# Optimization experiments

Hardware: AMD Instinct MI355X
Metric: run time of the kernel (lower is better)

Reference implementation:

```python
import jax, jax.numpy as jnp
import numpy as np

N_NODES = 100_000
N_EDGES = 1_600_000
F_NODE = 4
F_EDGE = 5
H = 64
EDGE_DIM = 2 * H + F_EDGE  # 133


def setup_inputs() -> dict:
    key = jax.random.key(0)
    ks = jax.random.split(key, 24)
    s = 0.05
    inp = {
        "node_feat": jax.random.normal(ks[0], (N_NODES, F_NODE), jnp.float32),
        "edge_feat": jax.random.normal(ks[1], (N_EDGES, F_EDGE), jnp.float32),
        "src": jax.random.randint(ks[2], (N_EDGES,), 0, N_NODES, jnp.int32),
        "dst": jax.random.randint(ks[3], (N_EDGES,), 0, N_NODES, jnp.int32),
        # SAGEConv 1 (DGL mean aggregator: fc_self(h) + fc_neigh(mean_neigh(h)) + bias)
        "W1s": jax.random.normal(ks[4], (F_NODE, H), jnp.float32) * s,
        "W1n": jax.random.normal(ks[5], (F_NODE, H), jnp.float32) * s,
        "b1": jnp.zeros((H,), jnp.float32),
        # SAGEConv 2
        "W2s": jax.random.normal(ks[6], (H, H), jnp.float32) * s,
        "W2n": jax.random.normal(ks[7], (H, H), jnp.float32) * s,
        "b2": jnp.zeros((H,), jnp.float32),
        # nodeprocess: Linear(F_NODE? no -> applied to h which is H-dim) Linear(H? )
        # NOTE: original declares nn.Linear(num_node_features, hidden) but applies it to h (H-dim);
        # we follow the applied shape, Linear(H, H), so the math is runnable and consistent.
        "Wnp": jax.random.normal(ks[8], (H, H), jnp.float32) * s,
        "bnp": jnp.zeros((H,), jnp.float32),
        # edgeprocess: Linear(EDGE_DIM, H) -> tanh -> Linear(H, 1)
        "We1": jax.random.normal(ks[9], (EDGE_DIM, H), jnp.float32) * s,
        "be1": jnp.zeros((H,), jnp.float32),
        "We2": jax.random.normal(ks[10], (H, 1), jnp.float32) * s,
        "be2": jnp.zeros((1,), jnp.float32),
        # lin1: Linear(EDGE_DIM, H); lin2: Linear(H, 1)
        "Wl1": jax.random.normal(ks[11], (EDGE_DIM, H), jnp.float32) * s,
        "bl1": jnp.zeros((H,), jnp.float32),
        "Wl2": jax.random.normal(ks[12], (H, 1), jnp.float32) * s,
        "bl2": jnp.zeros((1,), jnp.float32),
    }
    return inp


def _sage_mean(h, src, dst, Ws, Wn, b, inv_deg):
    # project first (cheaper: N x d instead of E x d), then gather+scatter-mean
    msg = (h @ Wn)[src]                                    # [E, H]
    agg = jax.ops.segment_sum(msg, dst, num_segments=h.shape[0]) * inv_deg
    return h @ Ws + agg + b


def reference(node_feat, edge_feat, src, dst,
              W1s, W1n, b1, W2s, W2n, b2,
              Wnp, bnp, We1, be1, We2, be2,
              Wl1, bl1, Wl2, bl2):
    n = node_feat.shape[0]
    deg = jax.ops.segment_sum(jnp.ones_like(dst, jnp.float32), dst, num_segments=n)
    inv_deg = (1.0 / jnp.maximum(deg, 1.0))[:, None]       # [N,1]

    h = jax.nn.relu(_sage_mean(node_feat, src, dst, W1s, W1n, b1, inv_deg))
    h = jax.nn.relu(_sage_mean(h, src, dst, W2s, W2n, b2, inv_deg))

    h_src = jax.nn.relu(h[src] @ Wnp + bnp)                # [E, H]
    h_dst = jax.nn.relu(h[dst] @ Wnp + bnp)                # [E, H]
    ef = jnp.concatenate([h_src, h_dst, edge_feat], axis=1)  # [E, 133]

    w = jax.nn.sigmoid(jnp.tanh(ef @ We1 + be1) @ We2 + be2)  # [E, 1]
    efw = ef * w
    out = jax.nn.relu(efw @ Wl1 + bl1)                     # dropout: eval mode (identity)
    return out @ Wl2 + bl2                                 # [E, 1]
```

## Files before the change

kernel.cpp:

```cpp
#include <hip/hip_runtime.h>
#include <math.h>


__device__ __forceinline__ float fast_tanh(float x) {
    x = fminf(fmaxf(x, -15.f), 15.f);
    float e2 = __expf(2.f * x);
    return (e2 - 1.f) * __builtin_amdgcn_rcpf(e2 + 1.f);
}
__device__ __forceinline__ float fast_sigmoid(float x) {
    x = fminf(fmaxf(x, -60.f), 60.f);
    return __builtin_amdgcn_rcpf(1.f + __expf(-x));
}
__device__ __forceinline__ unsigned short f2bf(float f) {
    unsigned u = __float_as_uint(f);
    u = u + 0x7FFFu + ((u >> 16) & 1u);
    return (unsigned short)(u >> 16);
}
__device__ __forceinline__ unsigned pack2bf(float lo, float hi) {
    return ((unsigned)f2bf(hi) << 16) | (unsigned)f2bf(lo);
}
__device__ __forceinline__ float bflo(unsigned u) { return __uint_as_float(u << 16); }
__device__ __forceinline__ float bfhi(unsigned u) { return __uint_as_float(u & 0xFFFF0000u); }

__device__ __forceinline__ float dpp_sum16(float x) {
    int t;
    t = __builtin_amdgcn_update_dpp(0, __float_as_int(x), 0xB1, 0xF, 0xF, true);
    x += __int_as_float(t);
    t = __builtin_amdgcn_update_dpp(0, __float_as_int(x), 0x4E, 0xF, 0xF, true);
    x += __int_as_float(t);
    t = __builtin_amdgcn_update_dpp(0, __float_as_int(x), 0x141, 0xF, 0xF, true);
    x += __int_as_float(t);
    t = __builtin_amdgcn_update_dpp(0, __float_as_int(x), 0x140, 0xF, 0xF, true);
    x += __int_as_float(t);
    return x;
}

__global__ void rank_k(const int* __restrict__ dst, int* __restrict__ deg,
                       int* __restrict__ rank, int E) {
    int e = blockIdx.x * blockDim.x + threadIdx.x;
    if (e < E) rank[e] = atomicAdd(&deg[dst[e]], 1);
}

__global__ void scan1_k(const int* __restrict__ deg, int* __restrict__ off,
                        int* __restrict__ bsum, int N) {
    __shared__ int tmp[256];
    int i = blockIdx.x * 256 + threadIdx.x;
    int v = (i < N) ? deg[i] : 0;
    tmp[threadIdx.x] = v;
    __syncthreads();
#pragma unroll
    for (int s = 1; s < 256; s <<= 1) {
        int t = (threadIdx.x >= s) ? tmp[threadIdx.x - s] : 0;
        __syncthreads();
        tmp[threadIdx.x] += t;
        __syncthreads();
    }
    if (i < N) off[i] = tmp[threadIdx.x] - v;
    if (threadIdx.x == 255) bsum[blockIdx.x] = tmp[255];
}

__global__ void scan2_k(int* __restrict__ bsum, int nb) {
    __shared__ int tmp[512];
    int i = threadIdx.x;
    int v = (i < nb) ? bsum[i] : 0;
    tmp[i] = v;
    __syncthreads();
#pragma unroll
    for (int s = 1; s < 512; s <<= 1) {
        int t = (i >= s) ? tmp[i - s] : 0;
        __syncthreads();
        tmp[i] += t;
        __syncthreads();
    }
    if (i < nb) bsum[i] = tmp[i] - v;
}

__global__ void scan3_k(int* __restrict__ off, const int* __restrict__ bsum,
                        int N, int E) {
    int i = blockIdx.x * 256 + threadIdx.x;
    if (i < N) off[i] += bsum[blockIdx.x];
    if (i == 0) off[N] = E;
}

__global__ void fill2_k(const int* __restrict__ src, const int* __restrict__ dst,
                        const int* __restrict__ off, const int* __restrict__ rank,
                        int2* __restrict__ csr, int E) {
    int e = blockIdx.x * blockDim.x + threadIdx.x;
    if (e >= E) return;
    csr[off[dst[e]] + rank[e]] = make_int2(src[e], e);
}

__global__ __launch_bounds__(256, 8)
void aggh1f_k(const int* __restrict__ off, const int2* __restrict__ csr,
              const float* __restrict__ nf,
              const float* __restrict__ W1s, const float* __restrict__ W1n,
              const float* __restrict__ b1, unsigned* __restrict__ h1b, int N) {
    int n = blockIdx.x * 16 + (threadIdx.x >> 4);
    if (n >= N) return;
    int q = threadIdx.x & 15;
    int s0 = off[n], s1 = off[n + 1];
    float4 a = {0.f, 0.f, 0.f, 0.f};
    for (int i = s0 + q; i < s1; i += 16) {
        float4 r = ((const float4*)nf)[csr[i].x];
        a.x += r.x; a.y += r.y; a.z += r.z; a.w += r.w;
    }
    a.x = dpp_sum16(a.x);
    a.y = dpp_sum16(a.y);
    a.z = dpp_sum16(a.z);
    a.w = dpp_sum16(a.w);
    float invd = 1.f / fmaxf((float)(s1 - s0), 1.f);
    a.x *= invd; a.y *= invd; a.z *= invd; a.w *= invd;
    float4 r = ((const float4*)nf)[n];
    const int j0 = q << 2;
    float4 acc = *(const float4*)&b1[j0];
#pragma unroll
    for (int k = 0; k < 4; ++k) {
        float rk = (k == 0) ? r.x : (k == 1) ? r.y : (k == 2) ? r.z : r.w;
        float ak = (k == 0) ? a.x : (k == 1) ? a.y : (k == 2) ? a.z : a.w;
        float4 ws = *(const float4*)&W1s[k * 64 + j0];
        float4 wn = *(const float4*)&W1n[k * 64 + j0];
        acc.x = fmaf(rk, ws.x, acc.x); acc.y = fmaf(rk, ws.y, acc.y);
        acc.z = fmaf(rk, ws.z, acc.z); acc.w = fmaf(rk, ws.w, acc.w);
        acc.x = fmaf(ak, wn.x, acc.x); acc.y = fmaf(ak, wn.y, acc.y);
        acc.z = fmaf(ak, wn.z, acc.z); acc.w = fmaf(ak, wn.w, acc.w);
    }
    uint2 pk;
    pk.x = pack2bf(fmaxf(acc.x, 0.f), fmaxf(acc.y, 0.f));
    pk.y = pack2bf(fmaxf(acc.z, 0.f), fmaxf(acc.w, 0.f));
    *(uint2*)&h1b[(size_t)n * 32 + (q << 1)] = pk;
}

__global__ __launch_bounds__(256, 8)
void gatherh1_k(const int* __restrict__ off, const int2* __restrict__ csr,
                const uint4* __restrict__ h1b4, uint4* __restrict__ ah1b4, int N) {
    int n = blockIdx.x * 4 + (threadIdx.x >> 6);
    if (n >= N) return;
    int l = threadIdx.x & 63;
    int g = l >> 3, q = l & 7;
    int s0 = off[n], s1 = off[n + 1];
    float a0 = 0.f, a1 = 0.f, a2 = 0.f, a3 = 0.f;
    float a4 = 0.f, a5 = 0.f, a6 = 0.f, a7 = 0.f;
    int i = s0;
    for (; i + 16 <= s1; i += 16) {
        int r0 = csr[i + g].x;
        int r1 = csr[i + 8 + g].x;
        uint4 v0 = h1b4[(size_t)r0 * 8 + q];
        uint4 v1 = h1b4[(size_t)r1 * 8 + q];
        a0 += bflo(v0.x) + bflo(v1.x); a1 += bfhi(v0.x) + bfhi(v1.x);
        a2 += bflo(v0.y) + bflo(v1.y); a3 += bfhi(v0.y) + bfhi(v1.y);
        a4 += bflo(v0.z) + bflo(v1.z); a5 += bfhi(v0.z) + bfhi(v1.z);
        a6 += bflo(v0.w) + bflo(v1.w); a7 += bfhi(v0.w) + bfhi(v1.w);
    }
    for (; i + 8 <= s1; i += 8) {
        int r = csr[i + g].x;
        uint4 v = h1b4[(size_t)r * 8 + q];
        a0 += bflo(v.x); a1 += bfhi(v.x);
        a2 += bflo(v.y); a3 += bfhi(v.y);
        a4 += bflo(v.z); a5 += bfhi(v.z);
        a6 += bflo(v.w); a7 += bfhi(v.w);
    }
    int rem = s1 - i;
    if (g < rem) {
        int r = csr[i + g].x;
        uint4 v = h1b4[(size_t)r * 8 + q];
        a0 += bflo(v.x); a1 += bfhi(v.x);
        a2 += bflo(v.y); a3 += bfhi(v.y);
        a4 += bflo(v.z); a5 += bfhi(v.z);
        a6 += bflo(v.w); a7 += bfhi(v.w);
    }
#pragma unroll
    for (int m = 8; m <= 32; m <<= 1) {
        a0 += __shfl_xor(a0, m); a1 += __shfl_xor(a1, m);
        a2 += __shfl_xor(a2, m); a3 += __shfl_xor(a3, m);
        a4 += __shfl_xor(a4, m); a5 += __shfl_xor(a5, m);
        a6 += __shfl_xor(a6, m); a7 += __shfl_xor(a7, m);
    }
    if (l < 8) {
        float invd = 1.f / fmaxf((float)(s1 - s0), 1.f);
        uint4 pk;
        pk.x = pack2bf(a0 * invd, a1 * invd);
        pk.y = pack2bf(a2 * invd, a3 * invd);
        pk.z = pack2bf(a4 * invd, a5 * invd);
        pk.w = pack2bf(a6 * invd, a7 * invd);
        ah1b4[(size_t)n * 8 + q] = pk;
    }
}

__device__ __forceinline__ void mac64(const float (*hT)[68], const float (*wt)[64],
                                      int rr, int cr, float acc[4][4]) {
#pragma unroll 8
    for (int k = 0; k < 64; ++k) {
        float4 a = *(const float4*)&hT[k][rr];
        float4 w = *(const float4*)&wt[k][cr];
        acc[0][0] = fmaf(a.x, w.x, acc[0][0]); acc[0][1] = fmaf(a.x, w.y, acc[0][1]);
        acc[0][2] = fmaf(a.x, w.z, acc[0][2]); acc[0][3] = fmaf(a.x, w.w, acc[0][3]);
        acc[1][0] = fmaf(a.y, w.x, acc[1][0]); acc[1][1] = fmaf(a.y, w.y, acc[1][1]);
        acc[1][2] = fmaf(a.y, w.z, acc[1][2]); acc[1][3] = fmaf(a.y, w.w, acc[1][3]);
        acc[2][0] = fmaf(a.z, w.x, acc[2][0]); acc[2][1] = fmaf(a.z, w.y, acc[2][1]);
        acc[2][2] = fmaf(a.z, w.z, acc[2][2]); acc[2][3] = fmaf(a.z, w.w, acc[2][3]);
        acc[3][0] = fmaf(a.w, w.x, acc[3][0]); acc[3][1] = fmaf(a.w, w.y, acc[3][1]);
        acc[3][2] = fmaf(a.w, w.z, acc[3][2]); acc[3][3] = fmaf(a.w, w.w, acc[3][3]);
    }
}

__global__ __launch_bounds__(256, 4)
void node_mlp_k(const unsigned* __restrict__ h1b, const unsigned* __restrict__ ah1b,
                const float* __restrict__ W2s, const float* __restrict__ W2n,
                const float* __restrict__ b2, const float* __restrict__ Wnp,
                const float* __restrict__ bnp, const float* __restrict__ We1,
                const float* __restrict__ Wl1, unsigned short* __restrict__ ST, int N) {
    __shared__ __align__(16) float hT[64][68];
    __shared__ __align__(16) float wt[64][64];
    const int t = threadIdx.x;
    const int m0 = blockIdx.x * 64;
    const int cr = (t & 15) << 2, rr = (t >> 4) << 2;
    float acc[4][4] = {};

#pragma unroll
    for (int it = 0; it < 8; ++it) {
        int u = it * 256 + t;
        int m = u >> 5, p = u & 31;
        int row = m0 + m;
        unsigned v = (row < N) ? h1b[(size_t)row * 32 + p] : 0u;
        hT[2 * p][m] = bflo(v);
        hT[2 * p + 1][m] = bfhi(v);
    }
#pragma unroll
    for (int it = 0; it < 16; ++it) {
        int k = it * 4 + (t >> 6), c = t & 63;
        wt[k][c] = W2s[k * 64 + c];
    }
    __syncthreads();
    mac64(hT, wt, rr, cr, acc);
    __syncthreads();

#pragma unroll
    for (int it = 0; it < 8; ++it) {
        int u = it * 256 + t;
        int m = u >> 5, p = u & 31;
        int row = m0 + m;
        unsigned v = (row < N) ? ah1b[(size_t)row * 32 + p] : 0u;
        hT[2 * p][m] = bflo(v);
        hT[2 * p + 1][m] = bfhi(v);
    }
#pragma unroll
    for (int it = 0; it < 16; ++it) {
        int k = it * 4 + (t >> 6), c = t & 63;
        wt[k][c] = W2n[k * 64 + c];
    }
    __syncthreads();
    mac64(hT, wt, rr, cr, acc);
    __syncthreads();

#pragma unroll
    for (int i = 0; i < 4; ++i)
#pragma unroll
        for (int q = 0; q < 4; ++q)
            hT[cr + q][rr + i] = fmaxf(acc[i][q] + b2[cr + q], 0.f);
#pragma unroll
    for (int it = 0; it < 16; ++it) {
        int k = it * 4 + (t >> 6), c = t & 63;
        wt[k][c] = Wnp[k * 64 + c];
    }
    __syncthreads();
    float ac2[4][4] = {};
    mac64(hT, wt, rr, cr, ac2);
    __syncthreads();

#pragma unroll
    for (int i = 0; i < 4; ++i)
#pragma unroll
        for (int q = 0; q < 4; ++q)
            hT[cr + q][rr + i] = fmaxf(ac2[i][q] + bnp[cr + q], 0.f);
    __syncthreads();

    for (int cb = 0; cb < 4; ++cb) {
        if (cb) __syncthreads();
#pragma unroll
        for (int it = 0; it < 16; ++it) {
            int k = it * 4 + (t >> 6), c = t & 63;
            int cglob = cb * 64 + c;
            int half = cglob >> 7, cc = cglob & 127;
            int jj = cc >> 1, p = cc & 1;
            const float* W = p ? Wl1 : We1;
            wt[k][c] = W[(half * 64 + k) * 64 + jj];
        }
        __syncthreads();
        float ac3[4][4] = {};
        mac64(hT, wt, rr, cr, ac3);
#pragma unroll
        for (int i = 0; i < 4; ++i) {
            int row = m0 + rr + i;
            if (row >= N) continue;
            ushort4 pk;
            pk.x = f2bf(ac3[i][0]); pk.y = f2bf(ac3[i][1]);
            pk.z = f2bf(ac3[i][2]); pk.w = f2bf(ac3[i][3]);
            *(ushort4*)&ST[(size_t)row * 256 + cb * 64 + cr] = pk;
        }
    }
}

__global__ void edge_k(const int2* __restrict__ csr, const int* __restrict__ dstarr,
                       const float* __restrict__ ef, const unsigned* __restrict__ ST32,
                       const float* __restrict__ We1, const float* __restrict__ be1,
                       const float* __restrict__ We2, const float* __restrict__ be2,
                       const float* __restrict__ Wl1, const float* __restrict__ bl1,
                       const float* __restrict__ Wl2, const float* __restrict__ bl2,
                       float* __restrict__ out, int E, int nwaves) {
    const int l = threadIdx.x & 63;
    const int g = l >> 4;
    const int q = l & 15;
    const int j0 = q << 2;
    const int wid = blockIdx.x * (blockDim.x >> 6) + (threadIdx.x >> 6);

    float4 wet[5], wlt[5];
#pragma unroll
    for (int k = 0; k < 5; ++k) {
        wet[k] = *(const float4*)&We1[(128 + k) * 64 + j0];
        wlt[k] = *(const float4*)&Wl1[(128 + k) * 64 + j0];
    }
    const float4 vbe1 = *(const float4*)&be1[j0];
    const float4 vwe2 = *(const float4*)&We2[j0];
    const float4 vbl1 = *(const float4*)&bl1[j0];
    const float4 vwl2 = *(const float4*)&Wl2[j0];
    const float vbe2 = be2[0], vbl2 = bl2[0];

    const int nch = (E + 3) >> 2;

#define KS(EK, K) \
    t4.x = fmaf(EK, wet[K].x, t4.x); t4.y = fmaf(EK, wet[K].y, t4.y); \
    t4.z = fmaf(EK, wet[K].z, t4.z); t4.w = fmaf(EK, wet[K].w, t4.w); \
    u4.x = fmaf(EK, wlt[K].x, u4.x); u4.y = fmaf(EK, wlt[K].y, u4.y); \
    u4.z = fmaf(EK, wlt[K].z, u4.z); u4.w = fmaf(EK, wlt[K].w, u4.w);

    for (int c = wid; c < nch; c += 2 * nwaves) {
        int c2 = c + nwaves;
        bool hasB = c2 < nch;
        int slotA = c * 4 + g;
        int slotB = hasB ? c2 * 4 + g : 0;
        bool actA = slotA < E;
        bool actB = hasB && slotB < E;
        int2 seA = csr[actA ? slotA : 0];
        int2 seB = csr[actB ? slotB : 0];
        int dnA = dstarr[seA.y];
        int dnB = dstarr[seB.y];
        uint4 pwA = *(const uint4*)&ST32[(size_t)dnA * 128 + 64 + j0];
        uint4 swA = *(const uint4*)&ST32[(size_t)seA.x * 128 + j0];
        uint4 pwB = *(const uint4*)&ST32[(size_t)dnB * 128 + 64 + j0];
        uint4 swB = *(const uint4*)&ST32[(size_t)seB.x * 128 + j0];
        const float* epA = ef + (size_t)seA.y * 5;
        const float* epB = ef + (size_t)seB.y * 5;
        float ekA0 = epA[0], ekA1 = epA[1], ekA2 = epA[2], ekA3 = epA[3], ekA4 = epA[4];
        float ekB0 = epB[0], ekB1 = epB[1], ekB2 = epB[2], ekB3 = epB[3], ekB4 = epB[4];

        {
            float4 t4 = {bflo(swA.x) + bflo(pwA.x) + vbe1.x,
                         bflo(swA.y) + bflo(pwA.y) + vbe1.y,
                         bflo(swA.z) + bflo(pwA.z) + vbe1.z,
                         bflo(swA.w) + bflo(pwA.w) + vbe1.w};
            float4 u4 = {bfhi(swA.x) + bfhi(pwA.x), bfhi(swA.y) + bfhi(pwA.y),
                         bfhi(swA.z) + bfhi(pwA.z), bfhi(swA.w) + bfhi(pwA.w)};
            KS(ekA0, 0) KS(ekA1, 1) KS(ekA2, 2) KS(ekA3, 3) KS(ekA4, 4)
            float z = fast_tanh(t4.x) * vwe2.x + fast_tanh(t4.y) * vwe2.y
                    + fast_tanh(t4.z) * vwe2.z + fast_tanh(t4.w) * vwe2.w;
            z = dpp_sum16(z);
            float w = fast_sigmoid(z + vbe2);
            float o = fmaxf(fmaf(w, u4.x, vbl1.x), 0.f) * vwl2.x
                    + fmaxf(fmaf(w, u4.y, vbl1.y), 0.f) * vwl2.y
                    + fmaxf(fmaf(w, u4.z, vbl1.z), 0.f) * vwl2.z
                    + fmaxf(fmaf(w, u4.w, vbl1.w), 0.f) * vwl2.w;
            o = dpp_sum16(o);
            if (q == 0 && actA) out[seA.y] = o + vbl2;
        }
        {
            float4 t4 = {bflo(swB.x) + bflo(pwB.x) + vbe1.x,
                         bflo(swB.y) + bflo(pwB.y) + vbe1.y,
                         bflo(swB.z) + bflo(pwB.z) + vbe1.z,
                         bflo(swB.w) + bflo(pwB.w) + vbe1.w};
            float4 u4 = {bfhi(swB.x) + bfhi(pwB.x), bfhi(swB.y) + bfhi(pwB.y),
                         bfhi(swB.z) + bfhi(pwB.z), bfhi(swB.w) + bfhi(pwB.w)};
            KS(ekB0, 0) KS(ekB1, 1) KS(ekB2, 2) KS(ekB3, 3) KS(ekB4, 4)
            float z = fast_tanh(t4.x) * vwe2.x + fast_tanh(t4.y) * vwe2.y
                    + fast_tanh(t4.z) * vwe2.z + fast_tanh(t4.w) * vwe2.w;
            z = dpp_sum16(z);
            float w = fast_sigmoid(z + vbe2);
            float o = fmaxf(fmaf(w, u4.x, vbl1.x), 0.f) * vwl2.x
                    + fmaxf(fmaf(w, u4.y, vbl1.y), 0.f) * vwl2.y
                    + fmaxf(fmaf(w, u4.z, vbl1.z), 0.f) * vwl2.z
                    + fmaxf(fmaf(w, u4.w, vbl1.w), 0.f) * vwl2.w;
            o = dpp_sum16(o);
            if (q == 0 && actB) out[seB.y] = o + vbl2;
        }
    }
#undef KS
}

extern "C" void kernel_launch(void* const* d_in, const int* in_sizes, int n_in,
                              void* d_out, int out_size, void* d_ws, size_t ws_size,
                              hipStream_t stream) {
    const float* nf  = (const float*)d_in[0];
    const float* ef  = (const float*)d_in[1];
    const int*   src = (const int*)d_in[2];
    const int*   dst = (const int*)d_in[3];
    const float* W1s = (const float*)d_in[4];
    const float* W1n = (const float*)d_in[5];
    const float* b1  = (const float*)d_in[6];
    const float* W2s = (const float*)d_in[7];
    const float* W2n = (const float*)d_in[8];
    const float* b2  = (const float*)d_in[9];
    const float* Wnp = (const float*)d_in[10];
    const float* bnp = (const float*)d_in[11];
    const float* We1 = (const float*)d_in[12];
    const float* be1 = (const float*)d_in[13];
    const float* We2 = (const float*)d_in[14];
    const float* be2 = (const float*)d_in[15];
    const float* Wl1 = (const float*)d_in[16];
    const float* bl1 = (const float*)d_in[17];
    const float* Wl2 = (const float*)d_in[18];
    const float* bl2 = (const float*)d_in[19];

    const int N = in_sizes[0] / 4;
    const int E = in_sizes[2];

    float* wsf = (float*)d_ws;
    unsigned short* ST = (unsigned short*)wsf;
    unsigned* ah1b = (unsigned*)(wsf + (size_t)128 * N);
    unsigned* h1b  = (unsigned*)(wsf + (size_t)192 * N);
    int2* csr  = (int2*)(wsf + (size_t)224 * N);
    int*  rank = (int*)(wsf + (size_t)256 * N);
    int*  deg  = (int*)(wsf + (size_t)272 * N);
    int*  off  = deg + N;
    int*  bsum = off + N + 1;
    float* out = (float*)d_out;

    const int nblkN1 = (N + 255) / 256;
    const int nblkE  = (E + 255) / 256;
    const int nblkNw4 = (N + 3) / 4;
    const int nblkN16 = (N + 15) / 16;
    const int gemmx  = (N + 63) / 64;
    const int EDGE_BLOCKS = 3072;
    const int nwaves = EDGE_BLOCKS * 4;

    hipMemsetAsync(deg, 0, (size_t)N * sizeof(int), stream);
    rank_k<<<nblkE, 256, 0, stream>>>(dst, deg, rank, E);
    scan1_k<<<nblkN1, 256, 0, stream>>>(deg, off, bsum, N);
    scan2_k<<<1, 512, 0, stream>>>(bsum, nblkN1);
    scan3_k<<<nblkN1, 256, 0, stream>>>(off, bsum, N, E);
    fill2_k<<<nblkE, 256, 0, stream>>>(src, dst, off, rank, csr, E);

    aggh1f_k<<<nblkN16, 256, 0, stream>>>(off, csr, nf, W1s, W1n, b1, h1b, N);

    gatherh1_k<<<nblkNw4, 256, 0, stream>>>(off, csr, (const uint4*)h1b,
                                            (uint4*)ah1b, N);

    node_mlp_k<<<gemmx, 256, 0, stream>>>(h1b, ah1b, W2s, W2n, b2,
                                          Wnp, bnp, We1, Wl1, ST, N);

    edge_k<<<EDGE_BLOCKS, 256, 0, stream>>>(csr, dst, ef, (const unsigned*)ST,
                                            We1, be1, We2, be2, Wl1, bl1, Wl2, bl2,
                                            out, E, nwaves);
}
```

Before: 505.3 us.

## Software-prefetch edge gathers, store CSR-ordered dst, fold be1 into node table

fill2_k now writes a dst array permuted into CSR order, so edge_k reads the destination node with a sequential load instead of a dependent random dst[e] lookup. edge_k restructures its loop to prefetch the next pair of edge chunks (indices, ST rows, edge features) while computing the current pair, to hide gather latency. The be1 bias is folded into the ST table in node_mlp_k, removing a per-edge add. Indexing switches from 64-bit size_t to 32-bit unsigned arithmetic; the costs are higher register pressure from the doubled prefetch state and extra workspace traffic for dstp.

```diff
diff --git a/kernel.cpp b/kernel.cpp
--- a/kernel.cpp
+++ b/kernel.cpp
@@ -84,10 +84,13 @@
 
 __global__ void fill2_k(const int* __restrict__ src, const int* __restrict__ dst,
                         const int* __restrict__ off, const int* __restrict__ rank,
-                        int2* __restrict__ csr, int E) {
+                        int2* __restrict__ csr, int* __restrict__ dstp, int E) {
     int e = blockIdx.x * blockDim.x + threadIdx.x;
     if (e >= E) return;
-    csr[off[dst[e]] + rank[e]] = make_int2(src[e], e);
+    int d = dst[e];
+    int pos = off[d] + rank[e];
+    csr[pos] = make_int2(src[e], e);
+    dstp[pos] = d;
 }
 
 __global__ __launch_bounds__(256, 8)
@@ -99,9 +102,10 @@
     if (n >= N) return;
     int q = threadIdx.x & 15;
     int s0 = off[n], s1 = off[n + 1];
+    const float4* nf4 = (const float4*)nf;
     float4 a = {0.f, 0.f, 0.f, 0.f};
     for (int i = s0 + q; i < s1; i += 16) {
-        float4 r = ((const float4*)nf)[csr[i].x];
+        float4 r = nf4[(unsigned)csr[i].x];
         a.x += r.x; a.y += r.y; a.z += r.z; a.w += r.w;
     }
     a.x = dpp_sum16(a.x);
@@ -110,7 +114,7 @@
     a.w = dpp_sum16(a.w);
     float invd = 1.f / fmaxf((float)(s1 - s0), 1.f);
     a.x *= invd; a.y *= invd; a.z *= invd; a.w *= invd;
-    float4 r = ((const float4*)nf)[n];
+    float4 r = nf4[(unsigned)n];
     const int j0 = q << 2;
     float4 acc = *(const float4*)&b1[j0];
 #pragma unroll
@@ -127,7 +131,7 @@
     uint2 pk;
     pk.x = pack2bf(fmaxf(acc.x, 0.f), fmaxf(acc.y, 0.f));
     pk.y = pack2bf(fmaxf(acc.z, 0.f), fmaxf(acc.w, 0.f));
-    *(uint2*)&h1b[(size_t)n * 32 + (q << 1)] = pk;
+    *(uint2*)&h1b[(unsigned)n * 32u + (q << 1)] = pk;
 }
 
 __global__ __launch_bounds__(256, 8)
@@ -144,8 +148,8 @@
     for (; i + 16 <= s1; i += 16) {
         int r0 = csr[i + g].x;
         int r1 = csr[i + 8 + g].x;
-        uint4 v0 = h1b4[(size_t)r0 * 8 + q];
-        uint4 v1 = h1b4[(size_t)r1 * 8 + q];
+        uint4 v0 = h1b4[(unsigned)r0 * 8u + q];
+        uint4 v1 = h1b4[(unsigned)r1 * 8u + q];
         a0 += bflo(v0.x) + bflo(v1.x); a1 += bfhi(v0.x) + bfhi(v1.x);
         a2 += bflo(v0.y) + bflo(v1.y); a3 += bfhi(v0.y) + bfhi(v1.y);
         a4 += bflo(v0.z) + bflo(v1.z); a5 += bfhi(v0.z) + bfhi(v1.z);
@@ -153,7 +157,7 @@
     }
     for (; i + 8 <= s1; i += 8) {
         int r = csr[i + g].x;
-        uint4 v = h1b4[(size_t)r * 8 + q];
+        uint4 v = h1b4[(unsigned)r * 8u + q];
         a0 += bflo(v.x); a1 += bfhi(v.x);
         a2 += bflo(v.y); a3 += bfhi(v.y);
         a4 += bflo(v.z); a5 += bfhi(v.z);
@@ -162,7 +166,7 @@
     int rem = s1 - i;
     if (g < rem) {
         int r = csr[i + g].x;
-        uint4 v = h1b4[(size_t)r * 8 + q];
+        uint4 v = h1b4[(unsigned)r * 8u + q];
         a0 += bflo(v.x); a1 += bfhi(v.x);
         a2 += bflo(v.y); a3 += bfhi(v.y);
         a4 += bflo(v.z); a5 += bfhi(v.z);
@@ -182,7 +186,7 @@
         pk.y = pack2bf(a2 * invd, a3 * invd);
         pk.z = pack2bf(a4 * invd, a5 * invd);
         pk.w = pack2bf(a6 * invd, a7 * invd);
-        ah1b4[(size_t)n * 8 + q] = pk;
+        ah1b4[(unsigned)n * 8u + q] = pk;
     }
 }
 
@@ -208,7 +212,8 @@
                 const float* __restrict__ W2s, const float* __restrict__ W2n,
                 const float* __restrict__ b2, const float* __restrict__ Wnp,
                 const float* __restrict__ bnp, const float* __restrict__ We1,
-                const float* __restrict__ Wl1, unsigned short* __restrict__ ST, int N) {
+                const float* __restrict__ Wl1, const float* __restrict__ be1,
+                unsigned short* __restrict__ ST, int N) {
     __shared__ __align__(16) float hT[64][68];
     __shared__ __align__(16) float wt[64][64];
     const int t = threadIdx.x;
@@ -221,7 +226,7 @@
         int u = it * 256 + t;
         int m = u >> 5, p = u & 31;
         int row = m0 + m;
-        unsigned v = (row < N) ? h1b[(size_t)row * 32 + p] : 0u;
+        unsigned v = (row < N) ? h1b[(unsigned)row * 32u + p] : 0u;
         hT[2 * p][m] = bflo(v);
         hT[2 * p + 1][m] = bfhi(v);
     }
@@ -239,7 +244,7 @@
         int u = it * 256 + t;
         int m = u >> 5, p = u & 31;
         int row = m0 + m;
-        unsigned v = (row < N) ? ah1b[(size_t)row * 32 + p] : 0u;
+        unsigned v = (row < N) ? ah1b[(unsigned)row * 32u + p] : 0u;
         hT[2 * p][m] = bflo(v);
         hT[2 * p + 1][m] = bfhi(v);
     }
@@ -288,21 +293,65 @@
         __syncthreads();
         float ac3[4][4] = {};
         mac64(hT, wt, rr, cr, ac3);
+        float bz0 = 0.f, bz2 = 0.f;
+        if (cb >= 2) {
+            int jj0 = ((cb * 64 + cr) & 127) >> 1;
+            bz0 = be1[jj0];
+            bz2 = be1[jj0 + 1];
+        }
 #pragma unroll
         for (int i = 0; i < 4; ++i) {
             int row = m0 + rr + i;
             if (row >= N) continue;
             ushort4 pk;
-            pk.x = f2bf(ac3[i][0]); pk.y = f2bf(ac3[i][1]);
-            pk.z = f2bf(ac3[i][2]); pk.w = f2bf(ac3[i][3]);
-            *(ushort4*)&ST[(size_t)row * 256 + cb * 64 + cr] = pk;
+            pk.x = f2bf(ac3[i][0] + bz0); pk.y = f2bf(ac3[i][1]);
+            pk.z = f2bf(ac3[i][2] + bz2); pk.w = f2bf(ac3[i][3]);
+            *(ushort4*)&ST[(unsigned)row * 256u + cb * 64 + cr] = pk;
         }
     }
 }
 
-__global__ void edge_k(const int2* __restrict__ csr, const int* __restrict__ dstarr,
+struct P8 {
+    int2 seA, seB;
+    int dnA, dnB;
+    uint4 pwA, swA, pwB, swB;
+    float eA0, eA1, eA2, eA3, eA4;
+    float eB0, eB1, eB2, eB3, eB4;
+    bool actA, actB;
+};
+
+__device__ __forceinline__ P8 pref_pair(int c, int nwaves, int nch, int E,
+                                        int g, int j0,
+                                        const int2* __restrict__ csr,
+                                        const int* __restrict__ dstp,
+                                        const float* __restrict__ ef,
+                                        const unsigned* __restrict__ ST32) {
+    P8 p;
+    int sA = c * 4 + g;
+    int cB = c + nwaves;
+    int sB = cB * 4 + g;
+    p.actA = (c < nch) && (sA < E);
+    p.actB = (cB < nch) && (sB < E);
+    unsigned uA = p.actA ? (unsigned)sA : 0u;
+    unsigned uB = p.actB ? (unsigned)sB : 0u;
+    p.dnA = dstp[uA];
+    p.dnB = dstp[uB];
+    p.seA = csr[uA];
+    p.seB = csr[uB];
+    p.pwA = *(const uint4*)&ST32[(unsigned)p.dnA * 128u + 64u + (unsigned)j0];
+    p.pwB = *(const uint4*)&ST32[(unsigned)p.dnB * 128u + 64u + (unsigned)j0];
+    p.swA = *(const uint4*)&ST32[(unsigned)p.seA.x * 128u + (unsigned)j0];
+    p.swB = *(const uint4*)&ST32[(unsigned)p.seB.x * 128u + (unsigned)j0];
+    const float* epA = ef + (unsigned)p.seA.y * 5u;
+    const float* epB = ef + (unsigned)p.seB.y * 5u;
+    p.eA0 = epA[0]; p.eA1 = epA[1]; p.eA2 = epA[2]; p.eA3 = epA[3]; p.eA4 = epA[4];
+    p.eB0 = epB[0]; p.eB1 = epB[1]; p.eB2 = epB[2]; p.eB3 = epB[3]; p.eB4 = epB[4];
+    return p;
+}
+
+__global__ void edge_k(const int2* __restrict__ csr, const int* __restrict__ dstp,
                        const float* __restrict__ ef, const unsigned* __restrict__ ST32,
-                       const float* __restrict__ We1, const float* __restrict__ be1,
+                       const float* __restrict__ We1,
                        const float* __restrict__ We2, const float* __restrict__ be2,
                        const float* __restrict__ Wl1, const float* __restrict__ bl1,
                        const float* __restrict__ Wl2, const float* __restrict__ bl2,
@@ -319,13 +368,13 @@
         wet[k] = *(const float4*)&We1[(128 + k) * 64 + j0];
         wlt[k] = *(const float4*)&Wl1[(128 + k) * 64 + j0];
     }
-    const float4 vbe1 = *(const float4*)&be1[j0];
     const float4 vwe2 = *(const float4*)&We2[j0];
     const float4 vbl1 = *(const float4*)&bl1[j0];
     const float4 vwl2 = *(const float4*)&Wl2[j0];
     const float vbe2 = be2[0], vbl2 = bl2[0];
 
     const int nch = (E + 3) >> 2;
+    const int step = 2 * nwaves;
 
 #define KS(EK, K) \
     t4.x = fmaf(EK, wet[K].x, t4.x); t4.y = fmaf(EK, wet[K].y, t4.y); \
@@ -333,34 +382,19 @@
     u4.x = fmaf(EK, wlt[K].x, u4.x); u4.y = fmaf(EK, wlt[K].y, u4.y); \
     u4.z = fmaf(EK, wlt[K].z, u4.z); u4.w = fmaf(EK, wlt[K].w, u4.w);
 
-    for (int c = wid; c < nch; c += 2 * nwaves) {
-        int c2 = c + nwaves;
-        bool hasB = c2 < nch;
-        int slotA = c * 4 + g;
-        int slotB = hasB ? c2 * 4 + g : 0;
-        bool actA = slotA < E;
-        bool actB = hasB && slotB < E;
-        int2 seA = csr[actA ? slotA : 0];
-        int2 seB = csr[actB ? slotB : 0];
-        int dnA = dstarr[seA.y];
-        int dnB = dstarr[seB.y];
-        uint4 pwA = *(const uint4*)&ST32[(size_t)dnA * 128 + 64 + j0];
-        uint4 swA = *(const uint4*)&ST32[(size_t)seA.x * 128 + j0];
-        uint4 pwB = *(const uint4*)&ST32[(size_t)dnB * 128 + 64 + j0];
-        uint4 swB = *(const uint4*)&ST32[(size_t)seB.x * 128 + j0];
-        const float* epA = ef + (size_t)seA.y * 5;
-        const float* epB = ef + (size_t)seB.y * 5;
-        float ekA0 = epA[0], ekA1 = epA[1], ekA2 = epA[2], ekA3 = epA[3], ekA4 = epA[4];
-        float ekB0 = epB[0], ekB1 = epB[1], ekB2 = epB[2], ekB3 = epB[3], ekB4 = epB[4];
+    P8 p = pref_pair(wid, nwaves, nch, E, g, j0, csr, dstp, ef, ST32);
+    for (int c = wid; c < nch; ) {
+        int cn = c + step;
+        P8 pn = pref_pair(cn, nwaves, nch, E, g, j0, csr, dstp, ef, ST32);
 
         {
-            float4 t4 = {bflo(swA.x) + bflo(pwA.x) + vbe1.x,
-                         bflo(swA.y) + bflo(pwA.y) + vbe1.y,
-                         bflo(swA.z) + bflo(pwA.z) + vbe1.z,
-                         bflo(swA.w) + bflo(pwA.w) + vbe1.w};
-            float4 u4 = {bfhi(swA.x) + bfhi(pwA.x), bfhi(swA.y) + bfhi(pwA.y),
-                         bfhi(swA.z) + bfhi(pwA.z), bfhi(swA.w) + bfhi(pwA.w)};
-            KS(ekA0, 0) KS(ekA1, 1) KS(ekA2, 2) KS(ekA3, 3) KS(ekA4, 4)
+            float4 t4 = {bflo(p.swA.x) + bflo(p.pwA.x),
+                         bflo(p.swA.y) + bflo(p.pwA.y),
+                         bflo(p.swA.z) + bflo(p.pwA.z),
+                         bflo(p.swA.w) + bflo(p.pwA.w)};
+            float4 u4 = {bfhi(p.swA.x) + bfhi(p.pwA.x), bfhi(p.swA.y) + bfhi(p.pwA.y),
+                         bfhi(p.swA.z) + bfhi(p.pwA.z), bfhi(p.swA.w) + bfhi(p.pwA.w)};
+            KS(p.eA0, 0) KS(p.eA1, 1) KS(p.eA2, 2) KS(p.eA3, 3) KS(p.eA4, 4)
             float z = fast_tanh(t4.x) * vwe2.x + fast_tanh(t4.y) * vwe2.y
                     + fast_tanh(t4.z) * vwe2.z + fast_tanh(t4.w) * vwe2.w;
             z = dpp_sum16(z);
@@ -370,16 +404,16 @@
                     + fmaxf(fmaf(w, u4.z, vbl1.z), 0.f) * vwl2.z
                     + fmaxf(fmaf(w, u4.w, vbl1.w), 0.f) * vwl2.w;
             o = dpp_sum16(o);
-            if (q == 0 && actA) out[seA.y] = o + vbl2;
+            if (q == 0 && p.actA) out[(unsigned)p.seA.y] = o + vbl2;
         }
         {
-            float4 t4 = {bflo(swB.x) + bflo(pwB.x) + vbe1.x,
-                         bflo(swB.y) + bflo(pwB.y) + vbe1.y,
-                         bflo(swB.z) + bflo(pwB.z) + vbe1.z,
-                         bflo(swB.w) + bflo(pwB.w) + vbe1.w};
-            float4 u4 = {bfhi(swB.x) + bfhi(pwB.x), bfhi(swB.y) + bfhi(pwB.y),
-                         bfhi(swB.z) + bfhi(pwB.z), bfhi(swB.w) + bfhi(pwB.w)};
-            KS(ekB0, 0) KS(ekB1, 1) KS(ekB2, 2) KS(ekB3, 3) KS(ekB4, 4)
+            float4 t4 = {bflo(p.swB.x) + bflo(p.pwB.x),
+                         bflo(p.swB.y) + bflo(p.pwB.y),
+                         bflo(p.swB.z) + bflo(p.pwB.z),
+                         bflo(p.swB.w) + bflo(p.pwB.w)};
+            float4 u4 = {bfhi(p.swB.x) + bfhi(p.pwB.x), bfhi(p.swB.y) + bfhi(p.pwB.y),
+                         bfhi(p.swB.z) + bfhi(p.pwB.z), bfhi(p.swB.w) + bfhi(p.pwB.w)};
+            KS(p.eB0, 0) KS(p.eB1, 1) KS(p.eB2, 2) KS(p.eB3, 3) KS(p.eB4, 4)
             float z = fast_tanh(t4.x) * vwe2.x + fast_tanh(t4.y) * vwe2.y
                     + fast_tanh(t4.z) * vwe2.z + fast_tanh(t4.w) * vwe2.w;
             z = dpp_sum16(z);
@@ -389,8 +423,10 @@
                     + fmaxf(fmaf(w, u4.z, vbl1.z), 0.f) * vwl2.z
                     + fmaxf(fmaf(w, u4.w, vbl1.w), 0.f) * vwl2.w;
             o = dpp_sum16(o);
-            if (q == 0 && actB) out[seB.y] = o + vbl2;
+            if (q == 0 && p.actB) out[(unsigned)p.seB.y] = o + vbl2;
         }
+        p = pn;
+        c = cn;
     }
 #undef KS
 }
@@ -425,6 +461,7 @@
     float* wsf = (float*)d_ws;
     unsigned short* ST = (unsigned short*)wsf;
     unsigned* ah1b = (unsigned*)(wsf + (size_t)128 * N);
+    int* dstp = (int*)(wsf + (size_t)160 * N);
     unsigned* h1b  = (unsigned*)(wsf + (size_t)192 * N);
     int2* csr  = (int2*)(wsf + (size_t)224 * N);
     int*  rank = (int*)(wsf + (size_t)256 * N);
@@ -446,7 +483,7 @@
     scan1_k<<<nblkN1, 256, 0, stream>>>(deg, off, bsum, N);
     scan2_k<<<1, 512, 0, stream>>>(bsum, nblkN1);
     scan3_k<<<nblkN1, 256, 0, stream>>>(off, bsum, N, E);
-    fill2_k<<<nblkE, 256, 0, stream>>>(src, dst, off, rank, csr, E);
+    fill2_k<<<nblkE, 256, 0, stream>>>(src, dst, off, rank, csr, dstp, E);
 
     aggh1f_k<<<nblkN16, 256, 0, stream>>>(off, csr, nf, W1s, W1n, b1, h1b, N);
 
@@ -454,9 +491,9 @@
                                             (uint4*)ah1b, N);
 
     node_mlp_k<<<gemmx, 256, 0, stream>>>(h1b, ah1b, W2s, W2n, b2,
-                                          Wnp, bnp, We1, Wl1, ST, N);
-
-    edge_k<<<EDGE_BLOCKS, 256, 0, stream>>>(csr, dst, ef, (const unsigned*)ST,
-                                            We1, be1, We2, be2, Wl1, bl1, Wl2, bl2,
+                                          Wnp, bnp, We1, Wl1, be1, ST, N);
+
+    edge_k<<<EDGE_BLOCKS, 256, 0, stream>>>(csr, dstp, ef, (const unsigned*)ST,
+                                            We1, We2, be2, Wl1, bl1, Wl2, bl2,
                                             out, E, nwaves);
 }
```

Result: no change. 502.3 us (-0.6%).
